# Kernel tuning notes

Hardware: AMD Instinct MI355X
Metric: run time of the kernel (lower is better)

Reference implementation:

```python
import jax, jax.numpy as jnp
import numpy as np

B, S, H, D, HID = 2, 4096, 16, 64, 1024
NUM_HASHES, CHUNK, NUM_BUCKETS = 2, 64, 128
N_BEFORE, N_AFTER = 1, 0
HASH_SEED = 0
SELF_MASK_VALUE = -1e5  # fp32 self-mask value from source buffers
EPS = 1e-6


def _look_adjacent(x, n_before, n_after):
    # x: [B,H,C,chunk,...]; concat chunks rolled along chunk axis (2) onto within-chunk axis (3)
    slices = [jnp.roll(x, -i, axis=2) for i in range(-n_before, n_after + 1)]
    return jnp.concatenate(slices, axis=3)


def _hash_vectors(vectors, rotations, num_buckets):
    # vectors: [B,H,S,D]; rotations: [H,D,NUM_HASHES,num_buckets//2] (shared q/k, seed reset in source)
    v = jax.lax.stop_gradient(vectors)  # vectors.detach() in source
    rotated = jnp.einsum('bhsd,hdnr->bhnsr', v, rotations)
    rotated = jnp.concatenate([rotated, -rotated], axis=-1)
    buckets = jnp.argmax(rotated, axis=-1)  # [B,H,NUM_HASHES,S]
    offsets = (jnp.arange(NUM_HASHES) * num_buckets).reshape(1, 1, -1, 1)
    return (buckets + offsets).reshape(vectors.shape[0], H, -1)  # [B,H,NUM_HASHES*S]


def _sorted_and_undo(buckets, seq_len):
    orig = jnp.arange(NUM_HASHES * seq_len) % seq_len
    scaled = seq_len * buckets + orig  # stable within-bucket ordering by position
    sorted_idx = jnp.argsort(scaled, axis=-1)
    undo_idx = jnp.argsort(sorted_idx, axis=-1)  # scatter-inverse of the sort
    return sorted_idx, undo_idx


def _len_and_dim_norm(x):
    var = jnp.mean(x * x, axis=-1, keepdims=True)
    return x * jax.lax.rsqrt(var + EPS) * np.float32(1.0 / np.sqrt(D))


def setup_inputs() -> dict:
    key = jax.random.key(0)
    k1, k2, k3, k4 = jax.random.split(key, 4)
    return {
        'decoder_states': jax.random.normal(k1, (B, S, HID), jnp.float32),
        'hidden_states': jax.random.normal(k2, (B, S, HID), jnp.float32),
        'w_qk': jax.random.normal(k3, (HID, H * D), jnp.float32) / np.float32(np.sqrt(HID)),
        'w_v': jax.random.normal(k4, (HID, H * D), jnp.float32) / np.float32(np.sqrt(HID)),
    }


def reference(decoder_states, hidden_states, w_qk, w_v):
    # projections (bias-free, Reformer-style), split heads -> [B,H,S,D]
    q = (decoder_states @ w_qk).reshape(B, S, H, D).transpose(0, 2, 1, 3)
    k = (hidden_states @ w_qk).reshape(B, S, H, D).transpose(0, 2, 1, 3)
    v = (hidden_states @ w_v).reshape(B, S, H, D).transpose(0, 2, 1, 3)

    rotations = jax.random.normal(jax.random.key(HASH_SEED),
                                  (H, D, NUM_HASHES, NUM_BUCKETS // 2), jnp.float32)
    q_buckets = _hash_vectors(q, rotations, NUM_BUCKETS)
    k_buckets = _hash_vectors(k, rotations, NUM_BUCKETS)
    sorted_q_idx, _ = _sorted_and_undo(q_buckets, S)
    sorted_k_idx, undo_k_idx = _sorted_and_undo(k_buckets, S)
    sorted_q_pos = sorted_q_idx % S
    sorted_k_pos = sorted_k_idx % S

    gather = lambda x, idx: jnp.take_along_axis(x, idx[..., None], axis=2)
    qs = gather(q, sorted_q_pos)  # [B,H,NUM_HASHES*S,D]
    ks = gather(k, sorted_k_pos)
    vs = gather(v, sorted_k_pos)

    n_chunks = NUM_HASHES * S // CHUNK
    to_chunks = lambda x: x.reshape(B, H, n_chunks, CHUNK, D)
    qs, ks, vs = to_chunks(qs), to_chunks(ks), to_chunks(vs)
    ks = _len_and_dim_norm(ks)

    ks = _look_adjacent(ks, N_BEFORE, N_AFTER)  # [B,H,C,2*CHUNK,D]
    vs = _look_adjacent(vs, N_BEFORE, N_AFTER)
    dots = jnp.einsum('bhcqd,bhckd->bhcqk', qs, ks)

    # self-mask: query position == adjacent key position (both from sorted QUERY idx, per source)
    q_idx = sorted_q_pos.reshape(B, H, n_chunks, CHUNK)
    kv_idx = _look_adjacent(q_idx, N_BEFORE, N_AFTER)  # [B,H,C,2*CHUNK]
    self_mask = q_idx[..., :, None] != kv_idx[..., None, :]
    dots = jnp.where(self_mask, dots, SELF_MASK_VALUE)

    logits = jax.nn.logsumexp(dots, axis=-1, keepdims=True)
    probs = jnp.exp(dots - logits)
    out = jnp.einsum('bhcqk,bhckd->bhcqd', probs, vs)

    out = out.reshape(B, H, NUM_HASHES * S, D)
    logits = logits.reshape(B, H, NUM_HASHES * S)
    # ReverseSort uses the KEY undo indices (as in source)
    out = jnp.take_along_axis(out, undo_k_idx[..., None], axis=2)
    logits = jnp.take_along_axis(logits, undo_k_idx, axis=2)

    # merge hash rounds via logsumexp weights (num_hashes > 1 branch)
    out = out.reshape(B, H, NUM_HASHES, S, D)
    logits = logits.reshape(B, H, NUM_HASHES, S, 1)
    w = jnp.exp(logits - jax.nn.logsumexp(logits, axis=2, keepdims=True))
    out = jnp.sum(out * w, axis=2)  # [B,H,S,D]
    return out.transpose(0, 2, 1, 3).reshape(B, S, H * D)
```

## Files before the change

### kernel.cpp

```cpp
#include <hip/hip_runtime.h>
#include <cstdint>
#include <cstddef>

#define BB 2
#define SS 4096
#define HH 16
#define DD 64
#define HID 1024
#define NHASH 2
#define CHUNK 64
#define NBUCK 128
#define NCHUNKS 128
#define NSORT 8192
#define BHN 32

#define KC_BLOCK 288

static constexpr size_t SZ_QKV  = (size_t)BB*HH*SS*DD*4;
static constexpr size_t OFF_Q   = 0;
static constexpr size_t OFF_K   = OFF_Q + SZ_QKV;
static constexpr size_t OFF_V   = OFF_K + SZ_QKV;
static constexpr size_t OFF_ROT = OFF_V + SZ_QKV;
static constexpr size_t OFF_QB  = OFF_ROT + (size_t)131072*4;
static constexpr size_t OFF_KB  = OFF_QB + (size_t)BHN*NSORT*4;
static constexpr size_t OFF_SQ  = OFF_KB + (size_t)BHN*NSORT*4;
static constexpr size_t OFF_SK  = OFF_SQ + (size_t)BHN*NSORT*4;
static constexpr size_t OFF_OUTR= OFF_SK + (size_t)BHN*NSORT*4;
static constexpr size_t OFF_LR  = OFF_OUTR + (size_t)BHN*NSORT*DD*4;
static constexpr size_t OFF_HBF = OFF_LR + (size_t)BHN*NSORT*4;
static constexpr size_t OFF_WBF = OFF_HBF + (size_t)8192*1024*2;
static constexpr size_t OFF_QBF = OFF_WBF + (size_t)1024*1024*2;
static constexpr size_t OFF_KBF = OFF_QBF + (size_t)BHN*SS*DD*2;
static constexpr size_t WS_REQUIRED = OFF_KBF + (size_t)BHN*SS*DD*2;

__device__ __forceinline__ float nofma_mul(float a, float b) {
  float r = a * b;
  asm("" : "+v"(r));
  return r;
}

__device__ __forceinline__ float xla_log1p_f32(float x) {
  float t = nofma_mul(-0.5f, x) + 1.0f;
  float small = nofma_mul(t, x);
  float onep = 1.0f + x;
  float big = (float)log((double)onep);
  return (fabsf(x) < 1e-4f) ? small : big;
}

__device__ __forceinline__ float erfinv_xla_f32(float x) {
  float nxx = -nofma_mul(x, x);
  float w = -xla_log1p_f32(nxx);
  float p;
  if (w < 5.0f) {
    float ww = w - 2.5f;
    p = 2.81022636e-08f;
    p = nofma_mul(p, ww) + 3.43273939e-07f;
    p = nofma_mul(p, ww) + -3.5233877e-06f;
    p = nofma_mul(p, ww) + -4.39150654e-06f;
    p = nofma_mul(p, ww) + 0.00021858087f;
    p = nofma_mul(p, ww) + -0.00125372503f;
    p = nofma_mul(p, ww) + -0.00417768164f;
    p = nofma_mul(p, ww) + 0.246640727f;
    p = nofma_mul(p, ww) + 1.50140941f;
  } else {
    float ww = sqrtf(w) - 3.0f;
    p = -0.000200214257f;
    p = nofma_mul(p, ww) + 0.000100950558f;
    p = nofma_mul(p, ww) + 0.00134934322f;
    p = nofma_mul(p, ww) + -0.00367342844f;
    p = nofma_mul(p, ww) + 0.00573950773f;
    p = nofma_mul(p, ww) + -0.0076224613f;
    p = nofma_mul(p, ww) + 0.00943887047f;
    p = nofma_mul(p, ww) + 1.00167406f;
    p = nofma_mul(p, ww) + 2.83297682f;
  }
  return nofma_mul(p, x);
}

__global__ void gen_rot_kernel(float* __restrict__ rot) {
  unsigned i = blockIdx.x * 256 + threadIdx.x;
  if (i >= 131072u) return;
  unsigned x0 = 0u, x1 = i;
  const unsigned ks2 = 0x1BD11BDAu;
#define TF_ROUND(r) { x0 += x1; x1 = (x1 << r) | (x1 >> (32 - r)); x1 ^= x0; }
  TF_ROUND(13) TF_ROUND(15) TF_ROUND(26) TF_ROUND(6)
              x1 += ks2 + 1u;
  TF_ROUND(17) TF_ROUND(29) TF_ROUND(16) TF_ROUND(24)
   x0 += ks2; x1 += 2u;
  TF_ROUND(13) TF_ROUND(15) TF_ROUND(26) TF_ROUND(6)
              x1 += 3u;
  TF_ROUND(17) TF_ROUND(29) TF_ROUND(16) TF_ROUND(24)
              x1 += ks2 + 4u;
  TF_ROUND(13) TF_ROUND(15) TF_ROUND(26) TF_ROUND(6)
   x0 += ks2; x1 += 5u;
#undef TF_ROUND
  unsigned bits = x0 ^ x1;
  float f = __uint_as_float(0x3f800000u | (bits >> 9)) - 1.0f;
  float u = f * 2.0f - 0.99999994f;
  u = fmaxf(-0.99999994f, u);
  rot[i] = nofma_mul(1.41421356f, erfinv_xla_f32(u));
}

__global__ __launch_bounds__(256) void gemm_kernel(const float* __restrict__ A,
                                                   const float* __restrict__ W,
                                                   float* __restrict__ dst) {
  __shared__ float As[32][132];
  __shared__ float Bs[32][68];
  const int m0 = blockIdx.x * 128;
  const int n0 = blockIdx.y * 64;
  const int tid = threadIdx.x;
  const int tr = tid >> 4, tc = tid & 15;
  float accT[8][4], acc[8][4];
#pragma unroll
  for (int i = 0; i < 8; ++i)
#pragma unroll
    for (int j2 = 0; j2 < 4; ++j2) { accT[i][j2] = 0.f; acc[i][j2] = 0.f; }

  float4 av[4], bv[2];
#pragma unroll
  for (int it = 0; it < 4; ++it) {
    int id = tid + it * 256;
    av[it] = *(const float4*)(A + (size_t)(m0 + (id >> 3)) * 1024 + ((id & 7) << 2));
  }
#pragma unroll
  for (int it = 0; it < 2; ++it) {
    int id = tid + it * 256;
    bv[it] = *(const float4*)(W + (size_t)(id >> 4) * 1024 + n0 + ((id & 15) << 2));
  }
  for (int kk = 0; kk < 1024; kk += 32) {
#pragma unroll
    for (int it = 0; it < 4; ++it) {
      int id = tid + it * 256;
      int m = id >> 3, kq = (id & 7) << 2;
      As[kq + 0][m] = av[it].x;
      As[kq + 1][m] = av[it].y;
      As[kq + 2][m] = av[it].z;
      As[kq + 3][m] = av[it].w;
    }
#pragma unroll
    for (int it = 0; it < 2; ++it) {
      int id = tid + it * 256;
      *(float4*)&Bs[id >> 4][(id & 15) << 2] = bv[it];
    }
    __syncthreads();
    if (kk + 32 < 1024) {
      int kn = kk + 32;
#pragma unroll
      for (int it = 0; it < 4; ++it) {
        int id = tid + it * 256;
        av[it] = *(const float4*)(A + (size_t)(m0 + (id >> 3)) * 1024 + kn + ((id & 7) << 2));
      }
#pragma unroll
      for (int it = 0; it < 2; ++it) {
        int id = tid + it * 256;
        bv[it] = *(const float4*)(W + (size_t)(kn + (id >> 4)) * 1024 + n0 + ((id & 15) << 2));
      }
    }
#pragma unroll
    for (int k = 0; k < 32; ++k) {
      float4 a0 = *(const float4*)&As[k][tr * 8];
      float4 a1 = *(const float4*)&As[k][tr * 8 + 4];
      float4 b0 = *(const float4*)&Bs[k][tc * 4];
      float a[8] = {a0.x, a0.y, a0.z, a0.w, a1.x, a1.y, a1.z, a1.w};
      float b[4] = {b0.x, b0.y, b0.z, b0.w};
#pragma unroll
      for (int i = 0; i < 8; ++i)
#pragma unroll
        for (int j2 = 0; j2 < 4; ++j2)
          acc[i][j2] = fmaf(a[i], b[j2], acc[i][j2]);
    }
    __syncthreads();
    if (((kk + 32) % KC_BLOCK) == 0) {
#pragma unroll
      for (int i = 0; i < 8; ++i)
#pragma unroll
        for (int j2 = 0; j2 < 4; ++j2) { accT[i][j2] += acc[i][j2]; acc[i][j2] = 0.f; }
    }
  }
#pragma unroll
  for (int i = 0; i < 8; ++i)
#pragma unroll
    for (int j2 = 0; j2 < 4; ++j2) accT[i][j2] += acc[i][j2];

  const int h = n0 >> 6;
  const int d = tc << 2;
#pragma unroll
  for (int i = 0; i < 8; ++i) {
    int m = m0 + tr * 8 + i;
    int b = m >> 12, s = m & 4095;
    float4 t = {accT[i][0], accT[i][1], accT[i][2], accT[i][3]};
    *(float4*)(dst + (((size_t)(b * 16 + h) * 4096 + s) << 6) + d) = t;
  }
}

__device__ __forceinline__ unsigned short f2bf(float f) {
  unsigned u = __float_as_uint(f);
  return (unsigned short)((u + 0x7fffu + ((u >> 16) & 1u)) >> 16);
}
__global__ void cast_bf16_kernel(const float* __restrict__ src,
                                 unsigned short* __restrict__ dst, int n4) {
  int i = blockIdx.x * 256 + threadIdx.x;
  if (i >= n4) return;
  float4 v = ((const float4*)src)[i];
  ushort4 o = {f2bf(v.x), f2bf(v.y), f2bf(v.z), f2bf(v.w)};
  ((ushort4*)dst)[i] = o;
}

typedef __attribute__((ext_vector_type(8))) short bf16x8;
typedef __attribute__((ext_vector_type(4))) float f32x4;

__global__ __launch_bounds__(256) void gemm_v_mfma(const unsigned short* __restrict__ Ab,
                                                   const unsigned short* __restrict__ Wb,
                                                   unsigned short* __restrict__ dst) {
  __shared__ unsigned short Bt[64][40];
  const int m0 = blockIdx.x * 64;
  const int n0 = blockIdx.y * 64;
  const int tid = threadIdx.x;
  const int w = tid >> 6, l = tid & 63;
  f32x4 acc[4];
#pragma unroll
  for (int fi = 0; fi < 4; ++fi) acc[fi] = {0.f, 0.f, 0.f, 0.f};

  const int arow = m0 + w * 16 + (l & 15);
  const int kgrp = (l >> 4) * 8;
  for (int kk = 0; kk < 1024; kk += 32) {
    {
      int k = tid >> 3, n8 = (tid & 7) * 8;
      bf16x8 v = *(const bf16x8*)(Wb + (size_t)(kk + k) * 1024 + n0 + n8);
#pragma unroll
      for (int i = 0; i < 8; ++i) Bt[n8 + i][k] = (unsigned short)v[i];
    }
    __syncthreads();
    bf16x8 a = *(const bf16x8*)(Ab + (size_t)arow * 1024 + kk + kgrp);
#pragma unroll
    for (int fi = 0; fi < 4; ++fi) {
      bf16x8 b = *(const bf16x8*)(&Bt[fi * 16 + (l & 15)][kgrp]);
      acc[fi] = __builtin_amdgcn_mfma_f32_16x16x32_bf16(a, b, acc[fi], 0, 0, 0);
    }
    __syncthreads();
  }
  const int h = n0 >> 6;
  const int mrow = m0 + w * 16 + (l >> 4) * 4;
#pragma unroll
  for (int fi = 0; fi < 4; ++fi) {
    int d = fi * 16 + (l & 15);
#pragma unroll
    for (int r = 0; r < 4; ++r) {
      int m = mrow + r;
      int b = m >> 12, s = m & 4095;
      dst[(((size_t)(b * 16 + h) * 4096 + s) << 6) + d] = f2bf(acc[fi][r]);
    }
  }
}

__global__ __launch_bounds__(128) void hash_kernel(const float* __restrict__ x,
                                                   const float* __restrict__ rot,
                                                   int* __restrict__ buck) {
  __shared__ float rs[8192];
  const int bh = blockIdx.y;
  const int h = bh & 15;
  const int s0 = blockIdx.x * 128;
  const int tid = threadIdx.x;
  for (int off = tid * 4; off < 8192; off += 512)
    *(float4*)&rs[off] = *(const float4*)(rot + (size_t)h * 8192 + off);
  __syncthreads();
  const int s = s0 + tid;
  const float* xr = x + ((size_t)bh * SS + s) * DD;
  float xv[64];
#pragma unroll
  for (int d4 = 0; d4 < 16; ++d4) {
    float4 t = *(const float4*)(xr + d4 * 4);
    xv[d4 * 4] = t.x; xv[d4 * 4 + 1] = t.y; xv[d4 * 4 + 2] = t.z; xv[d4 * 4 + 3] = t.w;
  }
#pragma unroll
  for (int n = 0; n < 2; ++n) {
    float acc[64];
#pragma unroll
    for (int r = 0; r < 64; ++r) acc[r] = 0.f;
#pragma unroll 2
    for (int d4 = 0; d4 < 16; ++d4) {
#pragma unroll
      for (int dd = 0; dd < 4; ++dd) {
        const float xd = xv[d4 * 4 + dd];
        const float* rp = rs + (d4 * 4 + dd) * 128 + n * 64;
#pragma unroll
        for (int r4 = 0; r4 < 16; ++r4) {
          float4 rv = *(const float4*)(rp + r4 * 4);
          acc[r4 * 4 + 0] = fmaf(xd, rv.x, acc[r4 * 4 + 0]);
          acc[r4 * 4 + 1] = fmaf(xd, rv.y, acc[r4 * 4 + 1]);
          acc[r4 * 4 + 2] = fmaf(xd, rv.z, acc[r4 * 4 + 2]);
          acc[r4 * 4 + 3] = fmaf(xd, rv.w, acc[r4 * 4 + 3]);
        }
      }
    }
    float best = -3.402823466e38f;
    int bi = 0;
#pragma unroll
    for (int idx = 0; idx < 128; ++idx) {
      float val = (idx < 64) ? acc[idx] : -acc[idx - 64];
      if (val > best) { best = val; bi = idx; }
    }
    buck[(size_t)bh * NSORT + n * SS + s] = bi + n * NBUCK;
  }
}

__global__ __launch_bounds__(256) void sort_kernel(const int* __restrict__ buck,
                                                   int* __restrict__ sorted) {
  const int bh = blockIdx.x >> 1;
  const int half = blockIdx.x & 1;
  const int* bk = buck + (size_t)bh * NSORT + half * SS;
  int* out = sorted + (size_t)bh * NSORT + half * SS;
  __shared__ int cnt[64][128];
  __shared__ int bl[SS];
  __shared__ int bbase[128];
  __shared__ int total[128];
  const int tid = threadIdx.x;
  for (int i = tid; i < 64 * 128; i += 256) (&cnt[0][0])[i] = 0;
  __syncthreads();
#pragma unroll
  for (int j = 0; j < 16; ++j) {
    int i = j * 256 + tid;
    int e = bk[i];
    bl[i] = e;
    atomicAdd(&cnt[i >> 6][e & 127], 1);
  }
  __syncthreads();
  if (tid < 128) {
    int s = 0;
#pragma unroll 4
    for (int c = 0; c < 64; ++c) {
      int t = cnt[c][tid];
      cnt[c][tid] = s;
      s += t;
    }
    total[tid] = s;
  }
  __syncthreads();
  if (tid == 0) {
    int s = 0;
#pragma unroll 4
    for (int v = 0; v < 128; ++v) { bbase[v] = s; s += total[v]; }
  }
  __syncthreads();
  if (tid < 64) {
    const int i0 = tid << 6;
    const int orig0 = half * SS + i0;
#pragma unroll 4
    for (int j = 0; j < 64; ++j) {
      int v = bl[i0 + j] & 127;
      int off = cnt[tid][v];
      cnt[tid][v] = off + 1;
      out[bbase[v] + off] = orig0 + j;
    }
  }
}

__global__ void undo_kernel(const int* __restrict__ srt, int* __restrict__ undo) {
  const int bh = blockIdx.x;
  for (int j = threadIdx.x; j < NSORT; j += 256)
    undo[(size_t)bh * NSORT + srt[(size_t)bh * NSORT + j]] = j;
}

__global__ __launch_bounds__(256) void attn_mfma_kernel(
    const unsigned short* __restrict__ qb16, const unsigned short* __restrict__ kb16,
    const unsigned short* __restrict__ vb16,
    const int* __restrict__ sq, const int* __restrict__ sk,
    float* __restrict__ outr, float* __restrict__ lr) {
  const int c = blockIdx.x, bh = blockIdx.y;
  const int cprev = (c + NCHUNKS - 1) & (NCHUNKS - 1);
  __shared__ unsigned short Qs[64][80];
  __shared__ unsigned short Ks[128][80];
  __shared__ unsigned short Vt[64][136];
  __shared__ unsigned short Ps[64][136];
  __shared__ int qpos[64];
  __shared__ int kvpos[128];
  __shared__ int krow[128];
  __shared__ float kscale[128];
  const int tid = threadIdx.x;
  const int* sqb = sq + (size_t)bh * NSORT;
  const int* skb = sk + (size_t)bh * NSORT;
  if (tid < 64) {
    int sqc = sqb[c * 64 + tid];
    int sqp = sqb[cprev * 64 + tid];
    qpos[tid] = sqc & (SS - 1);
    kvpos[tid] = sqp & (SS - 1);
    kvpos[64 + tid] = sqc & (SS - 1);
    krow[tid] = skb[cprev * 64 + tid] & (SS - 1);
    krow[64 + tid] = skb[c * 64 + tid] & (SS - 1);
  }
  __syncthreads();
  const unsigned short* kbase = kb16 + (size_t)bh * SS * DD;
  const unsigned short* vbase = vb16 + (size_t)bh * SS * DD;
  const unsigned short* qbase = qb16 + (size_t)bh * SS * DD;
#pragma unroll
  for (int it = 0; it < 4; ++it) {
    int id = tid + it * 256;
    int row = id >> 3, seg = id & 7;
    *(bf16x8*)&Ks[row][seg * 8] = *(const bf16x8*)(kbase + (size_t)krow[row] * DD + seg * 8);
  }
#pragma unroll
  for (int it = 0; it < 2; ++it) {
    int id = tid + it * 256;
    int row = id >> 3, seg = id & 7;
    *(bf16x8*)&Qs[row][seg * 8] = *(const bf16x8*)(qbase + (size_t)qpos[row] * DD + seg * 8);
  }
#pragma unroll
  for (int it = 0; it < 4; ++it) {
    int id = tid + it * 256;
    int col = id & 127, dg = id >> 7;
    bf16x8 v = *(const bf16x8*)(vbase + (size_t)krow[col] * DD + dg * 8);
#pragma unroll
    for (int i = 0; i < 8; ++i) Vt[dg * 8 + i][col] = (unsigned short)v[i];
  }
  __syncthreads();
  if (tid < 128) {
    float ss = 0.f;
#pragma unroll
    for (int seg = 0; seg < 8; ++seg) {
      bf16x8 t = *(const bf16x8*)&Ks[tid][seg * 8];
#pragma unroll
      for (int i = 0; i < 8; ++i) {
        float f = __uint_as_float(((unsigned)(unsigned short)t[i]) << 16);
        ss = fmaf(f, f, ss);
      }
    }
    kscale[tid] = rsqrtf(ss * (1.f / 64.f) + 1e-6f) * 0.125f;
  }
  __syncthreads();

  const int w = tid >> 6, l = tid & 63;
  const int lc = l & 15, lg = l >> 4;
  bf16x8 a0 = *(const bf16x8*)&Qs[w * 16 + lc][lg * 8];
  bf16x8 a1 = *(const bf16x8*)&Qs[w * 16 + lc][32 + lg * 8];
  f32x4 accs[8];
#pragma unroll
  for (int fi = 0; fi < 8; ++fi) {
    f32x4 acc = {0.f, 0.f, 0.f, 0.f};
    bf16x8 b0 = *(const bf16x8*)&Ks[fi * 16 + lc][lg * 8];
    bf16x8 b1 = *(const bf16x8*)&Ks[fi * 16 + lc][32 + lg * 8];
    acc = __builtin_amdgcn_mfma_f32_16x16x32_bf16(a0, b0, acc, 0, 0, 0);
    acc = __builtin_amdgcn_mfma_f32_16x16x32_bf16(a1, b1, acc, 0, 0, 0);
    accs[fi] = acc;
  }
  float kcs[8]; int kvp[8];
#pragma unroll
  for (int fi = 0; fi < 8; ++fi) { kcs[fi] = kscale[fi * 16 + lc]; kvp[fi] = kvpos[fi * 16 + lc]; }
  float ex[8][4], logit_r[4], seinv_r[4];
#pragma unroll
  for (int r = 0; r < 4; ++r) {
    const int qp = qpos[w * 16 + lg * 4 + r];
    float mr = -3.402823466e38f;
#pragma unroll
    for (int fi = 0; fi < 8; ++fi) {
      float d = accs[fi][r] * kcs[fi];
      if (qp == kvp[fi]) d = -1e5f;
      ex[fi][r] = d;
      mr = fmaxf(mr, d);
    }
    mr = fmaxf(mr, __shfl_xor(mr, 1));
    mr = fmaxf(mr, __shfl_xor(mr, 2));
    mr = fmaxf(mr, __shfl_xor(mr, 4));
    mr = fmaxf(mr, __shfl_xor(mr, 8));
    float s = 0.f;
#pragma unroll
    for (int fi = 0; fi < 8; ++fi) { float e = expf(ex[fi][r] - mr); ex[fi][r] = e; s += e; }
    s += __shfl_xor(s, 1);
    s += __shfl_xor(s, 2);
    s += __shfl_xor(s, 4);
    s += __shfl_xor(s, 8);
    logit_r[r] = mr + logf(s);
    seinv_r[r] = 1.f / s;
  }
#pragma unroll
  for (int r = 0; r < 4; ++r) {
    int row = w * 16 + lg * 4 + r;
#pragma unroll
    for (int fi = 0; fi < 8; ++fi)
      Ps[row][fi * 16 + lc] = f2bf(ex[fi][r]);
    if (lc == 0) lr[(size_t)bh * NSORT + c * 64 + row] = logit_r[r];
  }
  __syncthreads();
  f32x4 acco[4];
#pragma unroll
  for (int fi2 = 0; fi2 < 4; ++fi2) acco[fi2] = {0.f, 0.f, 0.f, 0.f};
#pragma unroll
  for (int kg = 0; kg < 4; ++kg) {
    bf16x8 a = *(const bf16x8*)&Ps[w * 16 + lc][kg * 32 + lg * 8];
#pragma unroll
    for (int fi2 = 0; fi2 < 4; ++fi2) {
      bf16x8 b = *(const bf16x8*)&Vt[fi2 * 16 + lc][kg * 32 + lg * 8];
      acco[fi2] = __builtin_amdgcn_mfma_f32_16x16x32_bf16(a, b, acco[fi2], 0, 0, 0);
    }
  }
#pragma unroll
  for (int fi2 = 0; fi2 < 4; ++fi2) {
    int d = fi2 * 16 + lc;
#pragma unroll
    for (int r = 0; r < 4; ++r) {
      int row = w * 16 + lg * 4 + r;
      outr[((size_t)bh * NSORT + c * 64 + row) * DD + d] = acco[fi2][r] * seinv_r[r];
    }
  }
}

__global__ void merge_kernel(const float* __restrict__ outr, const float* __restrict__ lr,
                             const int* __restrict__ undo, float* __restrict__ out) {
  const int idx = blockIdx.x * 256 + threadIdx.x;
  const int d4 = idx & 15;
  const int s = (idx >> 4) & (SS - 1);
  const int bh = idx >> 16;
  const int b = bh >> 4, h = bh & 15;
  const int u0 = undo[(size_t)bh * NSORT + s];
  const int u1 = undo[(size_t)bh * NSORT + SS + s];
  const float l0 = lr[(size_t)bh * NSORT + u0];
  const float l1 = lr[(size_t)bh * NSORT + u1];
  const float m = fmaxf(l0, l1);
  float w0 = expf(l0 - m), w1 = expf(l1 - m);
  const float inv = 1.f / (w0 + w1);
  w0 *= inv; w1 *= inv;
  const float4 r0 = *(const float4*)(outr + ((size_t)bh * NSORT + u0) * DD + d4 * 4);
  const float4 r1 = *(const float4*)(outr + ((size_t)bh * NSORT + u1) * DD + d4 * 4);
  float4 o;
  o.x = w0 * r0.x + w1 * r1.x;
  o.y = w0 * r0.y + w1 * r1.y;
  o.z = w0 * r0.z + w1 * r1.z;
  o.w = w0 * r0.w + w1 * r1.w;
  *(float4*)(out + ((size_t)(b * SS + s) * 1024) + h * 64 + d4 * 4) = o;
}

extern "C" void kernel_launch(void* const* d_in, const int* in_sizes, int n_in,
                              void* d_out, int out_size, void* d_ws, size_t ws_size,
                              hipStream_t stream) {
  if (ws_size < WS_REQUIRED) return;
  const float* dec = (const float*)d_in[0];
  const float* hid = (const float*)d_in[1];
  const float* wqk = (const float*)d_in[2];
  const float* wv  = (const float*)d_in[3];
  float* out = (float*)d_out;
  char* ws = (char*)d_ws;
  float* q    = (float*)(ws + OFF_Q);
  float* kk   = (float*)(ws + OFF_K);
  unsigned short* vbf = (unsigned short*)(ws + OFF_V);
  float* rotp = (float*)(ws + OFF_ROT);
  int*   qb   = (int*)(ws + OFF_QB);
  int*   kbk  = (int*)(ws + OFF_KB);
  int*   sqi  = (int*)(ws + OFF_SQ);
  int*   ski  = (int*)(ws + OFF_SK);
  float* outr = (float*)(ws + OFF_OUTR);
  float* lrp  = (float*)(ws + OFF_LR);
  unsigned short* hbf = (unsigned short*)(ws + OFF_HBF);
  unsigned short* wbf = (unsigned short*)(ws + OFF_WBF);
  unsigned short* qbf = (unsigned short*)(ws + OFF_QBF);
  unsigned short* kbf = (unsigned short*)(ws + OFF_KBF);

  gen_rot_kernel<<<512, 256, 0, stream>>>(rotp);
  cast_bf16_kernel<<<8192, 256, 0, stream>>>(hid, hbf, 8192 * 1024 / 4);
  cast_bf16_kernel<<<1024, 256, 0, stream>>>(wv, wbf, 1024 * 1024 / 4);
  gemm_kernel<<<dim3(64, 16), 256, 0, stream>>>(dec, wqk, q);
  gemm_kernel<<<dim3(64, 16), 256, 0, stream>>>(hid, wqk, kk);
  gemm_v_mfma<<<dim3(128, 16), 256, 0, stream>>>(hbf, wbf, vbf);
  hash_kernel<<<dim3(32, 32), 128, 0, stream>>>(q, rotp, qb);
  hash_kernel<<<dim3(32, 32), 128, 0, stream>>>(kk, rotp, kbk);
  cast_bf16_kernel<<<8192, 256, 0, stream>>>(q, qbf, 8192 * 1024 / 4);
  cast_bf16_kernel<<<8192, 256, 0, stream>>>(kk, kbf, 8192 * 1024 / 4);
  sort_kernel<<<64, 256, 0, stream>>>(qb, sqi);
  sort_kernel<<<64, 256, 0, stream>>>(kbk, ski);
  undo_kernel<<<32, 256, 0, stream>>>(ski, qb);
  attn_mfma_kernel<<<dim3(128, 32), 256, 0, stream>>>(qbf, kbf, vbf, sqi, ski, outr, lrp);
  merge_kernel<<<8192, 256, 0, stream>>>(outr, lrp, qb, out);
}
```

Measured before the change: 826.5 us.

## Fuse bf16 casts into GEMMs and fold undo-index computation into sort

The standalone bf16 cast kernels are removed. The Q/K GEMM epilogue now writes a bf16 copy next to the fp32 result, and the V MFMA GEMM converts its fp32 hidden-state and weight tiles to bf16 as it loads them. The sort kernel also writes the inverse permutation directly, which removes the separate undo kernel. This cuts several full-tensor read/write passes and kernel launches, at the cost of the V GEMM reading twice as many bytes per operand and doing redundant conversions.

```diff
diff --git a/kernel.cpp b/kernel.cpp
--- a/kernel.cpp
+++ b/kernel.cpp
@@ -27,9 +27,7 @@
 static constexpr size_t OFF_SK  = OFF_SQ + (size_t)BHN*NSORT*4;
 static constexpr size_t OFF_OUTR= OFF_SK + (size_t)BHN*NSORT*4;
 static constexpr size_t OFF_LR  = OFF_OUTR + (size_t)BHN*NSORT*DD*4;
-static constexpr size_t OFF_HBF = OFF_LR + (size_t)BHN*NSORT*4;
-static constexpr size_t OFF_WBF = OFF_HBF + (size_t)8192*1024*2;
-static constexpr size_t OFF_QBF = OFF_WBF + (size_t)1024*1024*2;
+static constexpr size_t OFF_QBF = OFF_LR + (size_t)BHN*NSORT*4;
 static constexpr size_t OFF_KBF = OFF_QBF + (size_t)BHN*SS*DD*2;
 static constexpr size_t WS_REQUIRED = OFF_KBF + (size_t)BHN*SS*DD*2;
 
@@ -101,9 +99,15 @@
   rot[i] = nofma_mul(1.41421356f, erfinv_xla_f32(u));
 }
 
+__device__ __forceinline__ unsigned short f2bf(float f) {
+  unsigned u = __float_as_uint(f);
+  return (unsigned short)((u + 0x7fffu + ((u >> 16) & 1u)) >> 16);
+}
+
 __global__ __launch_bounds__(256) void gemm_kernel(const float* __restrict__ A,
                                                    const float* __restrict__ W,
-                                                   float* __restrict__ dst) {
+                                                   float* __restrict__ dst,
+                                                   unsigned short* __restrict__ dstb) {
   __shared__ float As[32][132];
   __shared__ float Bs[32][68];
   const int m0 = blockIdx.x * 128;
@@ -188,29 +192,28 @@
   for (int i = 0; i < 8; ++i) {
     int m = m0 + tr * 8 + i;
     int b = m >> 12, s = m & 4095;
+    size_t base = (((size_t)(b * 16 + h) * 4096 + s) << 6) + d;
     float4 t = {accT[i][0], accT[i][1], accT[i][2], accT[i][3]};
-    *(float4*)(dst + (((size_t)(b * 16 + h) * 4096 + s) << 6) + d) = t;
-  }
-}
-
-__device__ __forceinline__ unsigned short f2bf(float f) {
-  unsigned u = __float_as_uint(f);
-  return (unsigned short)((u + 0x7fffu + ((u >> 16) & 1u)) >> 16);
-}
-__global__ void cast_bf16_kernel(const float* __restrict__ src,
-                                 unsigned short* __restrict__ dst, int n4) {
-  int i = blockIdx.x * 256 + threadIdx.x;
-  if (i >= n4) return;
-  float4 v = ((const float4*)src)[i];
-  ushort4 o = {f2bf(v.x), f2bf(v.y), f2bf(v.z), f2bf(v.w)};
-  ((ushort4*)dst)[i] = o;
+    *(float4*)(dst + base) = t;
+    ushort4 tb = {f2bf(t.x), f2bf(t.y), f2bf(t.z), f2bf(t.w)};
+    *(ushort4*)(dstb + base) = tb;
+  }
 }
 
 typedef __attribute__((ext_vector_type(8))) short bf16x8;
 typedef __attribute__((ext_vector_type(4))) float f32x4;
 
-__global__ __launch_bounds__(256) void gemm_v_mfma(const unsigned short* __restrict__ Ab,
-                                                   const unsigned short* __restrict__ Wb,
+__device__ __forceinline__ bf16x8 cvt8(float4 lo, float4 hi) {
+  bf16x8 r;
+  r[0] = (short)f2bf(lo.x); r[1] = (short)f2bf(lo.y);
+  r[2] = (short)f2bf(lo.z); r[3] = (short)f2bf(lo.w);
+  r[4] = (short)f2bf(hi.x); r[5] = (short)f2bf(hi.y);
+  r[6] = (short)f2bf(hi.z); r[7] = (short)f2bf(hi.w);
+  return r;
+}
+
+__global__ __launch_bounds__(256) void gemm_v_mfma(const float* __restrict__ Af,
+                                                   const float* __restrict__ Wf,
                                                    unsigned short* __restrict__ dst) {
   __shared__ unsigned short Bt[64][40];
   const int m0 = blockIdx.x * 64;
@@ -226,12 +229,14 @@
   for (int kk = 0; kk < 1024; kk += 32) {
     {
       int k = tid >> 3, n8 = (tid & 7) * 8;
-      bf16x8 v = *(const bf16x8*)(Wb + (size_t)(kk + k) * 1024 + n0 + n8);
+      const float* wp = Wf + (size_t)(kk + k) * 1024 + n0 + n8;
+      bf16x8 v = cvt8(*(const float4*)wp, *(const float4*)(wp + 4));
 #pragma unroll
       for (int i = 0; i < 8; ++i) Bt[n8 + i][k] = (unsigned short)v[i];
     }
     __syncthreads();
-    bf16x8 a = *(const bf16x8*)(Ab + (size_t)arow * 1024 + kk + kgrp);
+    const float* ap = Af + (size_t)arow * 1024 + kk + kgrp;
+    bf16x8 a = cvt8(*(const float4*)ap, *(const float4*)(ap + 4));
 #pragma unroll
     for (int fi = 0; fi < 4; ++fi) {
       bf16x8 b = *(const bf16x8*)(&Bt[fi * 16 + (l & 15)][kgrp]);
@@ -305,11 +310,13 @@
 }
 
 __global__ __launch_bounds__(256) void sort_kernel(const int* __restrict__ buck,
-                                                   int* __restrict__ sorted) {
+                                                   int* __restrict__ sorted,
+                                                   int* __restrict__ undo) {
   const int bh = blockIdx.x >> 1;
   const int half = blockIdx.x & 1;
   const int* bk = buck + (size_t)bh * NSORT + half * SS;
   int* out = sorted + (size_t)bh * NSORT + half * SS;
+  int* und = undo + (size_t)bh * NSORT;
   __shared__ int cnt[64][128];
   __shared__ int bl[SS];
   __shared__ int bbase[128];
@@ -350,15 +357,11 @@
       int v = bl[i0 + j] & 127;
       int off = cnt[tid][v];
       cnt[tid][v] = off + 1;
-      out[bbase[v] + off] = orig0 + j;
-    }
-  }
-}
-
-__global__ void undo_kernel(const int* __restrict__ srt, int* __restrict__ undo) {
-  const int bh = blockIdx.x;
-  for (int j = threadIdx.x; j < NSORT; j += 256)
-    undo[(size_t)bh * NSORT + srt[(size_t)bh * NSORT + j]] = j;
+      int pos = bbase[v] + off;
+      out[pos] = orig0 + j;
+      und[orig0 + j] = half * SS + pos;
+    }
+  }
 }
 
 __global__ __launch_bounds__(256) void attn_mfma_kernel(
@@ -548,24 +551,17 @@
   int*   ski  = (int*)(ws + OFF_SK);
   float* outr = (float*)(ws + OFF_OUTR);
   float* lrp  = (float*)(ws + OFF_LR);
-  unsigned short* hbf = (unsigned short*)(ws + OFF_HBF);
-  unsigned short* wbf = (unsigned short*)(ws + OFF_WBF);
   unsigned short* qbf = (unsigned short*)(ws + OFF_QBF);
   unsigned short* kbf = (unsigned short*)(ws + OFF_KBF);
 
   gen_rot_kernel<<<512, 256, 0, stream>>>(rotp);
-  cast_bf16_kernel<<<8192, 256, 0, stream>>>(hid, hbf, 8192 * 1024 / 4);
-  cast_bf16_kernel<<<1024, 256, 0, stream>>>(wv, wbf, 1024 * 1024 / 4);
-  gemm_kernel<<<dim3(64, 16), 256, 0, stream>>>(dec, wqk, q);
-  gemm_kernel<<<dim3(64, 16), 256, 0, stream>>>(hid, wqk, kk);
-  gemm_v_mfma<<<dim3(128, 16), 256, 0, stream>>>(hbf, wbf, vbf);
+  gemm_kernel<<<dim3(64, 16), 256, 0, stream>>>(dec, wqk, q, qbf);
+  gemm_kernel<<<dim3(64, 16), 256, 0, stream>>>(hid, wqk, kk, kbf);
+  gemm_v_mfma<<<dim3(128, 16), 256, 0, stream>>>(hid, wv, vbf);
   hash_kernel<<<dim3(32, 32), 128, 0, stream>>>(q, rotp, qb);
   hash_kernel<<<dim3(32, 32), 128, 0, stream>>>(kk, rotp, kbk);
-  cast_bf16_kernel<<<8192, 256, 0, stream>>>(q, qbf, 8192 * 1024 / 4);
-  cast_bf16_kernel<<<8192, 256, 0, stream>>>(kk, kbf, 8192 * 1024 / 4);
-  sort_kernel<<<64, 256, 0, stream>>>(qb, sqi);
-  sort_kernel<<<64, 256, 0, stream>>>(kbk, ski);
-  undo_kernel<<<32, 256, 0, stream>>>(ski, qb);
+  sort_kernel<<<64, 256, 0, stream>>>(qb, sqi, qb);
+  sort_kernel<<<64, 256, 0, stream>>>(kbk, ski, kbk);
   attn_mfma_kernel<<<dim3(128, 32), 256, 0, stream>>>(qbf, kbf, vbf, sqi, ski, outr, lrp);
-  merge_kernel<<<8192, 256, 0, stream>>>(outr, lrp, qb, out);
-}
+  merge_kernel<<<8192, 256, 0, stream>>>(outr, lrp, kbk, out);
+}
```

Measured after the change: 801.9 us. 3.0% less time.
